# Performance work log

Hardware: AMD Instinct MI355X
Metric: run time of the kernel (lower is better)

Reference implementation:

```python
import jax, jax.numpy as jnp
import numpy as np

N, E, G, ND, H, C, L = 100000, 640000, 1000, 128, 128, 10, 4
ATOMS_PER_GRAPH = 100  # N = G * ATOMS_PER_GRAPH
NEG_SLOPE = 0.01  # nn.LeakyReLU default


def setup_inputs() -> dict:
    key = jax.random.key(0)
    ks = jax.random.split(key, 16)
    s = 0.05
    return {
        "node_attr": jax.random.normal(ks[0], (N, ND), jnp.float32),
        "edge_index": jax.random.randint(ks[1], (2, E), 0, N, jnp.int64),
        "num_atoms": jnp.full((G,), ATOMS_PER_GRAPH, dtype=jnp.int64),
        "enc_W": jax.random.normal(ks[2], (ND, H), jnp.float32) * s,
        "enc_b": jnp.zeros((H,), jnp.float32),
        "gcn_W": jax.random.normal(ks[3], (L, H, H), jnp.float32) * s,
        "gcn_b": jnp.zeros((L, H), jnp.float32),
        "r_W1": jax.random.normal(ks[4], (H, H), jnp.float32) * s,
        "r_b1": jnp.zeros((H,), jnp.float32),
        "r_W2": jax.random.normal(ks[5], (H, H), jnp.float32) * s,
        "r_b2": jnp.zeros((H,), jnp.float32),
        "s_W1": jax.random.normal(ks[6], (H, H), jnp.float32) * s,
        "s_b1": jnp.zeros((H,), jnp.float32),
        "s_W2": jax.random.normal(ks[7], (H, H), jnp.float32) * s,
        "s_b2": jnp.zeros((H,), jnp.float32),
        "fin_W": jax.random.normal(ks[8], (H, C), jnp.float32) * s,
        "fin_b": jnp.zeros((C,), jnp.float32),
    }


def _leaky(x):
    return jnp.where(x > 0, x, NEG_SLOPE * x)


def reference(node_attr, edge_index, num_atoms, enc_W, enc_b, gcn_W, gcn_b,
              r_W1, r_b1, r_W2, r_b2, s_W1, s_b1, s_W2, s_b2, fin_W, fin_b):
    dst, src = edge_index[0], edge_index[1]
    # degree normalization constant across layers: deg(i) = in-edge count, divide by deg+1
    deg = jax.ops.segment_sum(jnp.ones((E,), node_attr.dtype), dst, num_segments=N)
    inv_deg = 1.0 / (deg + 1.0)  # [N]

    x = node_attr @ enc_W + enc_b  # [N, H]
    for l in range(L):
        h = x @ gcn_W[l] + gcn_b[l]
        agg = jax.ops.segment_sum(h[src], dst, num_segments=N)  # scatter_sum over dst
        x = (h + agg) * inv_deg[:, None]

    # GateMLP: ReLuMLP(x) * SigmoidMLP(x)
    r = _leaky(_leaky(x @ r_W1 + r_b1) @ r_W2 + r_b2)
    g = jax.nn.sigmoid(_leaky(x @ s_W1 + s_b1) @ s_W2 + s_b2)
    x = r * g  # [N, H]

    # graph pooling: scatter_mean over graph ids
    graph_mask = jnp.repeat(jnp.arange(G), num_atoms, total_repeat_length=N)
    gsum = jax.ops.segment_sum(x, graph_mask, num_segments=G)
    cnt = jax.ops.segment_sum(jnp.ones((N,), x.dtype), graph_mask, num_segments=G)
    graph_attr = gsum / jnp.maximum(cnt, 1.0)[:, None]  # [G, H]
    return graph_attr @ fin_W + fin_b  # [G, C]
```

## Files before the change

kernel.cpp:

```cpp
#include <hip/hip_runtime.h>
#include <hip/hip_bf16.h>
#include <cstddef>
#include <cstdint>

#define CAP 40
#define LEAK 0.01f

typedef __attribute__((ext_vector_type(8))) short short8v;
typedef __attribute__((ext_vector_type(4))) float float4v;

__device__ __forceinline__ unsigned short f2bf(float f) {
    uint32_t u = __float_as_uint(f);
    uint32_t r = (u + 0x7FFFu + ((u >> 16) & 1u)) >> 16;
    return (unsigned short)r;
}
__device__ __forceinline__ float bf2f(unsigned short s) {
    return __uint_as_float(((uint32_t)s) << 16);
}
__device__ __forceinline__ short8v frag_from_pairs(uint32_t p0, uint32_t p1,
                                                   uint32_t p2, uint32_t p3) {
    union { uint32_t u[4]; short8v v; } c;
    c.u[0] = p0; c.u[1] = p1; c.u[2] = p2; c.u[3] = p3;
    return c.v;
}

__global__ void build_buckets(const int* __restrict__ ei, int E_,
                              int* __restrict__ cnt, int* __restrict__ bucket) {
    int e = (blockIdx.x * 256 + threadIdx.x) * 4;
    if (e >= E_) return;
    if (e + 4 <= E_) {
        int4 d4 = *(const int4*)&ei[e];
        int4 s4 = *(const int4*)&ei[(size_t)E_ + e];
        int p0 = atomicAdd(&cnt[d4.x], 1);
        int p1 = atomicAdd(&cnt[d4.y], 1);
        int p2 = atomicAdd(&cnt[d4.z], 1);
        int p3 = atomicAdd(&cnt[d4.w], 1);
        if (p0 < CAP) bucket[(size_t)d4.x * CAP + p0] = s4.x;
        if (p1 < CAP) bucket[(size_t)d4.y * CAP + p1] = s4.y;
        if (p2 < CAP) bucket[(size_t)d4.z * CAP + p2] = s4.z;
        if (p3 < CAP) bucket[(size_t)d4.w * CAP + p3] = s4.w;
    } else {
        for (; e < E_; ++e) {
            int d = ei[e], s = ei[(size_t)E_ + e];
            int p = atomicAdd(&cnt[d], 1);
            if (p < CAP) bucket[(size_t)d * CAP + p] = s;
        }
    }
}

__global__ void pack_w(const float* __restrict__ enc, const float* __restrict__ gcn,
                       const float* __restrict__ rw1, const float* __restrict__ rw2,
                       const float* __restrict__ sw1, const float* __restrict__ sw2,
                       unsigned short* __restrict__ p) {
    int m = blockIdx.x >> 3;
    int idx = (blockIdx.x & 7) * 256 + threadIdx.x;
    const float* W;
    switch (m) {
        case 0: W = enc; break;
        case 1: case 2: case 3: case 4: W = gcn + (size_t)(m - 1) * 16384; break;
        case 5: W = rw1; break;
        case 6: W = rw2; break;
        case 7: W = sw1; break;
        default: W = sw2; break;
    }
    int n = idx & 127;
    int fg = (idx >> 7) & 3;
    int kc = idx >> 9;
    short8v v;
#pragma unroll
    for (int j = 0; j < 8; ++j)
        v[j] = (short)f2bf(W[(size_t)(kc * 32 + fg * 8 + j) * 128 + n]);
    *(short8v*)(p + (size_t)m * 16384 + (size_t)idx * 8) = v;
}

__device__ __forceinline__ void load_wf(const unsigned short* __restrict__ Wpack,
                                        int w, int fr, int fg, short8v wf[2][4]) {
    const short8v* Wp = (const short8v*)Wpack;
#pragma unroll
    for (int t = 0; t < 2; ++t)
#pragma unroll
        for (int kc = 0; kc < 4; ++kc)
            wf[t][kc] = Wp[(kc * 4 + fg) * 128 + w * 32 + t * 16 + fr];
}

__device__ __forceinline__ void mfma_tile(const unsigned short* As, int fr, int fg,
                                          const short8v wf[2][4], float4v acc[4][2]) {
#pragma unroll
    for (int m = 0; m < 4; ++m) {
        acc[m][0] = (float4v){0.f, 0.f, 0.f, 0.f};
        acc[m][1] = (float4v){0.f, 0.f, 0.f, 0.f};
    }
#pragma unroll
    for (int kc = 0; kc < 4; ++kc) {
        short8v a[4];
#pragma unroll
        for (int m = 0; m < 4; ++m) {
            int row = m * 16 + fr;
            int cb = (kc * 64 + fg * 16) ^ ((row & 7) << 4);
            a[m] = *(const short8v*)((const char*)As + row * 256 + cb);
        }
#pragma unroll
        for (int m = 0; m < 4; ++m) {
            acc[m][0] = __builtin_amdgcn_mfma_f32_16x16x32_bf16(a[m], wf[0][kc], acc[m][0], 0, 0, 0);
            acc[m][1] = __builtin_amdgcn_mfma_f32_16x16x32_bf16(a[m], wf[1][kc], acc[m][1], 0, 0, 0);
        }
    }
}

__global__ __launch_bounds__(256) void gemm_enc(const float* __restrict__ Ain,
                                                const unsigned short* __restrict__ Wpack,
                                                const float* __restrict__ bias,
                                                unsigned short* __restrict__ Cout, int M) {
    __shared__ unsigned short As[64 * 128];
    const int tid = threadIdx.x;
    const int lane = tid & 63;
    const int w = tid >> 6;
    const int row0 = blockIdx.x * 64;
    const int fr = lane & 15;
    const int fg = lane >> 4;

    short8v wf[2][4];
    load_wf(Wpack, w, fr, fg, wf);

    {
        const int r = tid >> 2;
        const int cg = tid & 3;
        const int row = row0 + r;
        char* lbase = (char*)As + r * 256;
        const float* Ap = Ain + (size_t)row * 128 + cg * 32;
#pragma unroll
        for (int i = 0; i < 4; ++i) {
            short8v v = {0, 0, 0, 0, 0, 0, 0, 0};
            if (row < M) {
                float4v p = *(const float4v*)(Ap + i * 8);
                float4v q = *(const float4v*)(Ap + i * 8 + 4);
                v[0] = (short)f2bf(p[0]); v[1] = (short)f2bf(p[1]);
                v[2] = (short)f2bf(p[2]); v[3] = (short)f2bf(p[3]);
                v[4] = (short)f2bf(q[0]); v[5] = (short)f2bf(q[1]);
                v[6] = (short)f2bf(q[2]); v[7] = (short)f2bf(q[3]);
            }
            int cb = (cg * 64 + i * 16) ^ ((r & 7) << 4);
            *(short8v*)(lbase + cb) = v;
        }
    }
    __syncthreads();

    float4v acc[4][2];
    mfma_tile(As, fr, fg, wf, acc);

#pragma unroll
    for (int t = 0; t < 2; ++t) {
        const int col = w * 32 + t * 16 + fr;
        const float bv = bias[col];
#pragma unroll
        for (int m = 0; m < 4; ++m)
#pragma unroll
            for (int q = 0; q < 4; ++q) {
                int row = row0 + m * 16 + fg * 4 + q;
                if (row < M) Cout[(size_t)row * 128 + col] = f2bf(acc[m][t][q] + bv);
            }
    }
}

__device__ __forceinline__ void acc8(float a[8], uint4 v, float m) {
    a[0] = fmaf(m, bf2f((unsigned short)(v.x & 0xffff)), a[0]);
    a[1] = fmaf(m, bf2f((unsigned short)(v.x >> 16)), a[1]);
    a[2] = fmaf(m, bf2f((unsigned short)(v.y & 0xffff)), a[2]);
    a[3] = fmaf(m, bf2f((unsigned short)(v.y >> 16)), a[3]);
    a[4] = fmaf(m, bf2f((unsigned short)(v.z & 0xffff)), a[4]);
    a[5] = fmaf(m, bf2f((unsigned short)(v.z >> 16)), a[5]);
    a[6] = fmaf(m, bf2f((unsigned short)(v.w & 0xffff)), a[6]);
    a[7] = fmaf(m, bf2f((unsigned short)(v.w >> 16)), a[7]);
}

__global__ __launch_bounds__(256, 4) void gcn_fused(const unsigned short* __restrict__ x,
                                                    const int* __restrict__ bucket,
                                                    const int* __restrict__ cnt,
                                                    const unsigned short* __restrict__ Wpack,
                                                    const float* __restrict__ bias,
                                                    unsigned short* __restrict__ xout,
                                                    int Nn) {
    __shared__ unsigned short As[64 * 128];
    const int tid = threadIdx.x;
    const int lane = tid & 63;
    const int w = tid >> 6;
    const int row0 = blockIdx.x * 64;
    const int fr = lane & 15;
    const int fg = lane >> 4;
    const int l16 = lane & 15;
    const int g = lane >> 4;
    const int gl = lane & 48;
    const char* xb = (const char*)x;

    int cfull = 0;
    if (lane < 16) {
        int gn = row0 + w * 16 + lane;
        if (gn >= Nn) gn = Nn - 1;
        cfull = cnt[gn];
    }
    uint4 own[4];
    int2 pre[4];
#pragma unroll
    for (int p = 0; p < 4; ++p) {
        int gn = row0 + w * 16 + p * 4 + g;
        if (gn >= Nn) gn = Nn - 1;
        own[p] = *(const uint4*)(xb + (size_t)gn * 256 + l16 * 16);
        pre[p] = *(const int2*)&bucket[(size_t)gn * CAP + 2 * l16];
    }

#pragma unroll
    for (int p = 0; p < 4; ++p) {
        const int n = p * 4 + g;
        const int r = w * 16 + n;
        const int dfull = __shfl(cfull, n);
        const float id = 1.0f / (float)(dfull + 1);
        const int d = min(dfull, CAP);
        const int dm = min(d, 32);

        float a[8];
        {
            uint4 o = own[p];
            a[0] = bf2f((unsigned short)(o.x & 0xffff));
            a[1] = bf2f((unsigned short)(o.x >> 16));
            a[2] = bf2f((unsigned short)(o.y & 0xffff));
            a[3] = bf2f((unsigned short)(o.y >> 16));
            a[4] = bf2f((unsigned short)(o.z & 0xffff));
            a[5] = bf2f((unsigned short)(o.z >> 16));
            a[6] = bf2f((unsigned short)(o.w & 0xffff));
            a[7] = bf2f((unsigned short)(o.w >> 16));
        }

        for (int j = 0; j < dm; j += 4) {
            int sl = gl + (j >> 1);
            int s0 = __shfl(pre[p].x, sl);
            int s1 = __shfl(pre[p].y, sl);
            int s2 = __shfl(pre[p].x, sl + 1);
            int s3 = __shfl(pre[p].y, sl + 1);
            s0 = min(max(s0, 0), Nn - 1);
            s1 = min(max(s1, 0), Nn - 1);
            s2 = min(max(s2, 0), Nn - 1);
            s3 = min(max(s3, 0), Nn - 1);
            uint4 v0 = *(const uint4*)(xb + (size_t)s0 * 256 + l16 * 16);
            uint4 v1 = *(const uint4*)(xb + (size_t)s1 * 256 + l16 * 16);
            uint4 v2 = *(const uint4*)(xb + (size_t)s2 * 256 + l16 * 16);
            uint4 v3 = *(const uint4*)(xb + (size_t)s3 * 256 + l16 * 16);
            acc8(a, v0, (j + 0 < d) ? 1.f : 0.f);
            acc8(a, v1, (j + 1 < d) ? 1.f : 0.f);
            acc8(a, v2, (j + 2 < d) ? 1.f : 0.f);
            acc8(a, v3, (j + 3 < d) ? 1.f : 0.f);
        }
        if (d > 32) {
            int gn = row0 + r; if (gn >= Nn) gn = Nn - 1;
            for (int j = 32; j < d; ++j) {
                int s = bucket[(size_t)gn * CAP + j];
                uint4 v = *(const uint4*)(xb + (size_t)s * 256 + l16 * 16);
                acc8(a, v, 1.f);
            }
        }

#pragma unroll
        for (int i = 0; i < 8; ++i) a[i] *= id;
        uint4 o;
        o.x = (uint32_t)f2bf(a[0]) | ((uint32_t)f2bf(a[1]) << 16);
        o.y = (uint32_t)f2bf(a[2]) | ((uint32_t)f2bf(a[3]) << 16);
        o.z = (uint32_t)f2bf(a[4]) | ((uint32_t)f2bf(a[5]) << 16);
        o.w = (uint32_t)f2bf(a[6]) | ((uint32_t)f2bf(a[7]) << 16);
        *(uint4*)((char*)As + r * 256 + ((l16 * 16) ^ ((r & 7) << 4))) = o;
    }

    short8v wf[2][4];
    load_wf(Wpack, w, fr, fg, wf);
    __syncthreads();

    float4v acc[4][2];
    mfma_tile(As, fr, fg, wf, acc);

#pragma unroll
    for (int t = 0; t < 2; ++t) {
        const int col = w * 32 + t * 16 + fr;
        const float bv = bias[col];
#pragma unroll
        for (int m = 0; m < 4; ++m)
#pragma unroll
            for (int q = 0; q < 4; ++q) {
                int row = row0 + m * 16 + fg * 4 + q;
                if (row < Nn) xout[(size_t)row * 128 + col] = f2bf(acc[m][t][q] + bv);
            }
    }
}

__global__ __launch_bounds__(512, 4) void gate_fused(const unsigned short* __restrict__ x,
                                                     const unsigned short* __restrict__ wpack,
                                                     const float* __restrict__ rb1,
                                                     const float* __restrict__ rb2,
                                                     const float* __restrict__ sb1,
                                                     const float* __restrict__ sb2,
                                                     unsigned short* __restrict__ out, int M) {
    __shared__ unsigned short Ws[2 * 128 * 128];
    const int tid = threadIdx.x;
    const int lane = tid & 63;
    const int w = tid >> 6;
    const int l16 = lane & 15;
    const int fg = lane >> 4;
    const int row0 = blockIdx.x * 128 + w * 16;

    int xr = row0 + l16;
    if (xr >= M) xr = M - 1;
    short8v xbf[4];
#pragma unroll
    for (int kc = 0; kc < 4; ++kc)
        xbf[kc] = *(const short8v*)(x + (size_t)xr * 128 + kc * 32 + fg * 8);

    const short8v* WL = (const short8v*)Ws;
    uint32_t upR[8][2], upS[8][2];

#define STAGE2(mi0, mi1)                                                      \
    {                                                                         \
        const short8v* s0 = (const short8v*)(wpack + (size_t)(mi0) * 16384);  \
        const short8v* s1 = (const short8v*)(wpack + (size_t)(mi1) * 16384);  \
        short8v* dst = (short8v*)Ws;                                          \
        _Pragma("unroll") for (int i = 0; i < 4; ++i)                         \
            dst[i * 512 + tid] = s0[i * 512 + tid];                           \
        _Pragma("unroll") for (int i = 0; i < 4; ++i)                         \
            dst[2048 + i * 512 + tid] = s1[i * 512 + tid];                    \
    }

#define PASS1(OFS, BIAS, UP)                                                  \
    _Pragma("unroll") for (int nt = 0; nt < 8; ++nt) {                        \
        float4v acc = (float4v){0.f, 0.f, 0.f, 0.f};                          \
        _Pragma("unroll") for (int kc = 0; kc < 4; ++kc)                      \
            acc = __builtin_amdgcn_mfma_f32_16x16x32_bf16(                    \
                WL[(OFS) + (kc * 4 + fg) * 128 + nt * 16 + l16], xbf[kc], acc, 0, 0, 0); \
        _Pragma("unroll") for (int q = 0; q < 4; ++q) {                       \
            float v = acc[q] + (BIAS)[nt * 16 + fg * 4 + q];                  \
            acc[q] = v > 0.f ? v : LEAK * v;                                  \
        }                                                                     \
        UP[nt][0] = (uint32_t)f2bf(acc[0]) | ((uint32_t)f2bf(acc[1]) << 16);  \
        UP[nt][1] = (uint32_t)f2bf(acc[2]) | ((uint32_t)f2bf(acc[3]) << 16);  \
    }

#define MKUF(UP, UF)                                                          \
    _Pragma("unroll") for (int kc = 0; kc < 4; ++kc) {                        \
        uint32_t pr0, pr1, pr2, pr3;                                          \
        {                                                                     \
            int srcl = (((2 * fg + 0) & 3) << 4) + l16;                       \
            uint32_t lo = __shfl((int)UP[2 * kc][0], srcl);                   \
            uint32_t hi = __shfl((int)UP[2 * kc + 1][0], srcl);               \
            pr0 = (fg & 2) ? hi : lo;                                         \
            lo = __shfl((int)UP[2 * kc][1], srcl);                            \
            hi = __shfl((int)UP[2 * kc + 1][1], srcl);                        \
            pr1 = (fg & 2) ? hi : lo;                                         \
        }                                                                     \
        {                                                                     \
            int srcl = (((2 * fg + 1) & 3) << 4) + l16;                       \
            uint32_t lo = __shfl((int)UP[2 * kc][0], srcl);                   \
            uint32_t hi = __shfl((int)UP[2 * kc + 1][0], srcl);               \
            pr2 = (fg & 2) ? hi : lo;                                         \
            lo = __shfl((int)UP[2 * kc][1], srcl);                            \
            hi = __shfl((int)UP[2 * kc + 1][1], srcl);                        \
            pr3 = (fg & 2) ? hi : lo;                                         \
        }                                                                     \
        UF[kc] = frag_from_pairs(pr0, pr1, pr2, pr3);                         \
    }

    STAGE2(5, 7);
    __syncthreads();
    PASS1(0, rb1, upR);
    PASS1(2048, sb1, upS);
    __syncthreads();

    STAGE2(6, 8);
    __syncthreads();

    short8v uf[4];
    MKUF(upR, uf);
    float4v rf[8];
#pragma unroll
    for (int t2 = 0; t2 < 8; ++t2) {
        float4v acc = (float4v){0.f, 0.f, 0.f, 0.f};
#pragma unroll
        for (int kc = 0; kc < 4; ++kc)
            acc = __builtin_amdgcn_mfma_f32_16x16x32_bf16(
                uf[kc], WL[(kc * 4 + fg) * 128 + t2 * 16 + l16], acc, 0, 0, 0);
        const float bv = rb2[t2 * 16 + l16];
#pragma unroll
        for (int q = 0; q < 4; ++q) {
            float v = acc[q] + bv;
            rf[t2][q] = v > 0.f ? v : LEAK * v;
        }
    }

    MKUF(upS, uf);
#pragma unroll
    for (int t2 = 0; t2 < 8; ++t2) {
        float4v acc = (float4v){0.f, 0.f, 0.f, 0.f};
#pragma unroll
        for (int kc = 0; kc < 4; ++kc)
            acc = __builtin_amdgcn_mfma_f32_16x16x32_bf16(
                uf[kc], WL[2048 + (kc * 4 + fg) * 128 + t2 * 16 + l16], acc, 0, 0, 0);
        const float bv = sb2[t2 * 16 + l16];
#pragma unroll
        for (int q = 0; q < 4; ++q) {
            int row = row0 + fg * 4 + q;
            if (row < M) {
                float gg = 1.f / (1.f + __expf(-(acc[q] + bv)));
                out[(size_t)row * 128 + t2 * 16 + l16] = f2bf(gg * rf[t2][q]);
            }
        }
    }
#undef STAGE2
#undef PASS1
#undef MKUF
}

__global__ void scan_atoms(const int* __restrict__ na, int* __restrict__ goff, int G_) {
    __shared__ int sh[1024];
    int t = threadIdx.x;
    int v = (t < G_) ? na[t] : 0;
    sh[t] = v;
    __syncthreads();
    for (int ofs = 1; ofs < 1024; ofs <<= 1) {
        int u = (t >= ofs) ? sh[t - ofs] : 0;
        __syncthreads();
        sh[t] += u;
        __syncthreads();
    }
    if (t == 0) goff[0] = 0;
    if (t < G_) goff[t + 1] = sh[t];
}

__global__ void pool(const unsigned short* __restrict__ x, const int* __restrict__ goff,
                     float* __restrict__ gattr, int G_) {
    int g = blockIdx.x * 2 + (threadIdx.x >> 7);
    if (g >= G_) return;
    int d = threadIdx.x & 127;
    int a0 = goff[g], a1 = goff[g + 1];
    float s0 = 0.f, s1 = 0.f, s2 = 0.f, s3 = 0.f;
    int a = a0;
    for (; a + 4 <= a1; a += 4) {
        s0 += bf2f(x[(size_t)(a + 0) * 128 + d]);
        s1 += bf2f(x[(size_t)(a + 1) * 128 + d]);
        s2 += bf2f(x[(size_t)(a + 2) * 128 + d]);
        s3 += bf2f(x[(size_t)(a + 3) * 128 + d]);
    }
    for (; a < a1; ++a) s0 += bf2f(x[(size_t)a * 128 + d]);
    float s = (s0 + s1) + (s2 + s3);
    float c = (float)max(a1 - a0, 1);
    gattr[(size_t)g * 128 + d] = s / c;
}

__global__ void final_gemm(const float* __restrict__ gattr, const float* __restrict__ fW,
                           const float* __restrict__ fb, float* __restrict__ out,
                           int G_, int C_) {
    int i = blockIdx.x * 256 + threadIdx.x;
    if (i >= G_ * C_) return;
    int g = i / C_, c = i % C_;
    const float* row = gattr + (size_t)g * 128;
    float s = fb[c];
    for (int k = 0; k < 128; ++k) s = fmaf(row[k], fW[k * C_ + c], s);
    out[i] = s;
}

extern "C" void kernel_launch(void* const* d_in, const int* in_sizes, int n_in,
                              void* d_out, int out_size, void* d_ws, size_t ws_size,
                              hipStream_t stream) {
    const float* node_attr = (const float*)d_in[0];
    const int* edge_index  = (const int*)d_in[1];
    const int* num_atoms   = (const int*)d_in[2];
    const float* enc_W = (const float*)d_in[3];
    const float* enc_b = (const float*)d_in[4];
    const float* gcn_W = (const float*)d_in[5];
    const float* gcn_b = (const float*)d_in[6];
    const float* r_W1 = (const float*)d_in[7];
    const float* r_b1 = (const float*)d_in[8];
    const float* r_W2 = (const float*)d_in[9];
    const float* r_b2 = (const float*)d_in[10];
    const float* s_W1 = (const float*)d_in[11];
    const float* s_b1 = (const float*)d_in[12];
    const float* s_W2 = (const float*)d_in[13];
    const float* s_b2 = (const float*)d_in[14];
    const float* fin_W = (const float*)d_in[15];
    const float* fin_b = (const float*)d_in[16];
    float* out = (float*)d_out;

    const int N_ = in_sizes[0] / 128;
    const int E_ = in_sizes[1] / 2;
    const int G_ = in_sizes[2];
    const int C_ = in_sizes[16];

    size_t off = 0;
    auto alloc = [&](size_t bytes) -> void* {
        void* p = (char*)d_ws + off;
        off += (bytes + 255) & ~(size_t)255;
        return p;
    };
    unsigned short* bx = (unsigned short*)alloc((size_t)N_ * 128 * 2);
    unsigned short* bh = (unsigned short*)alloc((size_t)N_ * 128 * 2);
    int* bucket = (int*)alloc((size_t)N_ * CAP * 4);
    int* cnt    = (int*)alloc((size_t)N_ * 4);
    unsigned short* wpack = (unsigned short*)alloc((size_t)9 * 16384 * 2);
    int* goff   = (int*)alloc((size_t)(G_ + 1) * 4);
    float* gattr = (float*)alloc((size_t)G_ * 128 * 4);
    (void)ws_size; (void)n_in; (void)out_size;

    const int gemm_grid = (N_ + 63) / 64;

    hipMemsetAsync(cnt, 0, (size_t)N_ * 4, stream);
    build_buckets<<<(E_ / 4 + 255) / 256, 256, 0, stream>>>(edge_index, E_, cnt, bucket);
    pack_w<<<72, 256, 0, stream>>>(enc_W, gcn_W, r_W1, r_W2, s_W1, s_W2, wpack);
    scan_atoms<<<1, 1024, 0, stream>>>(num_atoms, goff, G_);

    gemm_enc<<<gemm_grid, 256, 0, stream>>>(node_attr, wpack, enc_b, bx, N_);

    unsigned short* cur = bx;
    unsigned short* nxt = bh;
    for (int l = 0; l < 4; ++l) {
        gcn_fused<<<gemm_grid, 256, 0, stream>>>(cur, bucket, cnt,
                                                 wpack + (size_t)(1 + l) * 16384,
                                                 gcn_b + (size_t)l * 128, nxt, N_);
        unsigned short* t = cur; cur = nxt; nxt = t;
    }

    gate_fused<<<(N_ + 127) / 128, 512, 0, stream>>>(cur, wpack, r_b1, r_b2, s_b1, s_b2,
                                                     nxt, N_);

    pool<<<(G_ + 1) / 2, 256, 0, stream>>>(nxt, goff, gattr, G_);
    final_gemm<<<(G_ * C_ + 255) / 256, 256, 0, stream>>>(gattr, fin_W, fin_b, out, G_, C_);
}
```

Measured before the change: 297.5 us.

## Fold encoder and last GCN weights into adjacent GEMMs, merge prep kernels

Aggregation and degree normalisation are linear, so they commute with the right-multiply by the weights. This change folds the encoder weight into the first GCN layer weight, and the last GCN weight into the first gate-MLP weights, with the biases folded to match. The encoder GEMM kernel goes away, and the last GCN layer only aggregates before writing. Bucket building, node_attr bf16 conversion, weight packing and the small weight-product matmuls now run in one combined prep launch. The cost is extra prep work and bf16 rounding of the products, which changes numerics slightly.

```diff
diff --git a/kernel.cpp b/kernel.cpp
--- a/kernel.cpp
+++ b/kernel.cpp
@@ -24,53 +24,113 @@
     return c.v;
 }
 
-__global__ void build_buckets(const int* __restrict__ ei, int E_,
-                              int* __restrict__ cnt, int* __restrict__ bucket) {
-    int e = (blockIdx.x * 256 + threadIdx.x) * 4;
-    if (e >= E_) return;
-    if (e + 4 <= E_) {
-        int4 d4 = *(const int4*)&ei[e];
-        int4 s4 = *(const int4*)&ei[(size_t)E_ + e];
-        int p0 = atomicAdd(&cnt[d4.x], 1);
-        int p1 = atomicAdd(&cnt[d4.y], 1);
-        int p2 = atomicAdd(&cnt[d4.z], 1);
-        int p3 = atomicAdd(&cnt[d4.w], 1);
-        if (p0 < CAP) bucket[(size_t)d4.x * CAP + p0] = s4.x;
-        if (p1 < CAP) bucket[(size_t)d4.y * CAP + p1] = s4.y;
-        if (p2 < CAP) bucket[(size_t)d4.z * CAP + p2] = s4.z;
-        if (p3 < CAP) bucket[(size_t)d4.w * CAP + p3] = s4.w;
-    } else {
-        for (; e < E_; ++e) {
-            int d = ei[e], s = ei[(size_t)E_ + e];
-            int p = atomicAdd(&cnt[d], 1);
-            if (p < CAP) bucket[(size_t)d * CAP + p] = s;
-        }
-    }
-}
-
-__global__ void pack_w(const float* __restrict__ enc, const float* __restrict__ gcn,
-                       const float* __restrict__ rw1, const float* __restrict__ rw2,
-                       const float* __restrict__ sw1, const float* __restrict__ sw2,
-                       unsigned short* __restrict__ p) {
-    int m = blockIdx.x >> 3;
-    int idx = (blockIdx.x & 7) * 256 + threadIdx.x;
-    const float* W;
-    switch (m) {
-        case 0: W = enc; break;
-        case 1: case 2: case 3: case 4: W = gcn + (size_t)(m - 1) * 16384; break;
-        case 5: W = rw1; break;
-        case 6: W = rw2; break;
-        case 7: W = sw1; break;
-        default: W = sw2; break;
-    }
-    int n = idx & 127;
-    int fg = (idx >> 7) & 3;
-    int kc = idx >> 9;
-    short8v v;
-#pragma unroll
-    for (int j = 0; j < 8; ++j)
-        v[j] = (short)f2bf(W[(size_t)(kc * 32 + fg * 8 + j) * 128 + n]);
-    *(short8v*)(p + (size_t)m * 16384 + (size_t)idx * 8) = v;
+__global__ __launch_bounds__(256) void prep(const int* __restrict__ ei, int E_,
+                                            int* __restrict__ cnt,
+                                            int* __restrict__ bucket,
+                                            const float* __restrict__ node_attr,
+                                            unsigned short* __restrict__ bx, int Nn,
+                                            const float* __restrict__ enc_W,
+                                            const float* __restrict__ gcn_W,
+                                            const float* __restrict__ rw1,
+                                            const float* __restrict__ rw2,
+                                            const float* __restrict__ sw1,
+                                            const float* __restrict__ sw2,
+                                            const float* __restrict__ enc_b,
+                                            const float* __restrict__ gcn_b,
+                                            const float* __restrict__ rb1,
+                                            const float* __restrict__ sb1,
+                                            unsigned short* __restrict__ wpack,
+                                            float* __restrict__ fbias,
+                                            int NB_EDGE, int NB_CVT) {
+    const int b = blockIdx.x;
+    const int tid = threadIdx.x;
+
+    if (b < NB_EDGE) {
+        int e = (b * 256 + tid) * 4;
+        if (e >= E_) return;
+        if (e + 4 <= E_) {
+            int4 d4 = *(const int4*)&ei[e];
+            int4 s4 = *(const int4*)&ei[(size_t)E_ + e];
+            int p0 = atomicAdd(&cnt[d4.x], 1);
+            int p1 = atomicAdd(&cnt[d4.y], 1);
+            int p2 = atomicAdd(&cnt[d4.z], 1);
+            int p3 = atomicAdd(&cnt[d4.w], 1);
+            if (p0 < CAP) bucket[(size_t)d4.x * CAP + p0] = s4.x;
+            if (p1 < CAP) bucket[(size_t)d4.y * CAP + p1] = s4.y;
+            if (p2 < CAP) bucket[(size_t)d4.z * CAP + p2] = s4.z;
+            if (p3 < CAP) bucket[(size_t)d4.w * CAP + p3] = s4.w;
+        } else {
+            for (; e < E_; ++e) {
+                int d = ei[e], s = ei[(size_t)E_ + e];
+                int p = atomicAdd(&cnt[d], 1);
+                if (p < CAP) bucket[(size_t)d * CAP + p] = s;
+            }
+        }
+        return;
+    }
+    if (b < NB_EDGE + NB_CVT) {
+        size_t i8 = ((size_t)(b - NB_EDGE) * 256 + tid) * 8;
+        if (i8 < (size_t)Nn * 128) {
+            const float* ap = node_attr + i8;
+            float4v p = *(const float4v*)ap;
+            float4v q = *(const float4v*)(ap + 4);
+            short8v v;
+            v[0] = (short)f2bf(p[0]); v[1] = (short)f2bf(p[1]);
+            v[2] = (short)f2bf(p[2]); v[3] = (short)f2bf(p[3]);
+            v[4] = (short)f2bf(q[0]); v[5] = (short)f2bf(q[1]);
+            v[6] = (short)f2bf(q[2]); v[7] = (short)f2bf(q[3]);
+            *(short8v*)(bx + i8) = v;
+        }
+        return;
+    }
+    if (b < NB_EDGE + NB_CVT + 72) {
+        int pb = b - (NB_EDGE + NB_CVT);
+        int m = pb >> 3;
+        if (m == 1) return;
+        int idx = (pb & 7) * 256 + tid;
+        const float* W;
+        switch (m) {
+            case 0: W = enc_W; break;
+            case 2: case 3: case 4: W = gcn_W + (size_t)(m - 1) * 16384; break;
+            case 5: W = rw1; break;
+            case 6: W = rw2; break;
+            case 7: W = sw1; break;
+            default: W = sw2; break;
+        }
+        int n = idx & 127;
+        int fg = (idx >> 7) & 3;
+        int kc = idx >> 9;
+        short8v v;
+#pragma unroll
+        for (int j = 0; j < 8; ++j)
+            v[j] = (short)f2bf(W[(size_t)(kc * 32 + fg * 8 + j) * 128 + n]);
+        *(short8v*)(wpack + (size_t)m * 16384 + (size_t)idx * 8) = v;
+        return;
+    }
+    int fb = b - (NB_EDGE + NB_CVT + 72);
+    if (fb < 192) {
+        int which = fb / 64;
+        int r = (fb % 64) * 2 + (tid >> 7);
+        int n = tid & 127;
+        const float* A = (which == 0) ? enc_W : gcn_W + (size_t)3 * 16384;
+        const float* B = (which == 0) ? gcn_W : ((which == 1) ? rw1 : sw1);
+        float acc = 0.f;
+#pragma unroll 8
+        for (int m2 = 0; m2 < 128; ++m2)
+            acc = fmaf(A[(size_t)r * 128 + m2], B[(size_t)m2 * 128 + n], acc);
+        int kc = r >> 5, fg2 = (r >> 3) & 3, j = r & 7;
+        int sl = (which == 0) ? 1 : ((which == 1) ? 9 : 10);
+        wpack[(size_t)sl * 16384 + (size_t)(((kc * 4 + fg2) * 128 + n) * 8 + j)] = f2bf(acc);
+    } else if (fb < 195 && tid < 128) {
+        int which = fb - 192;
+        const float* B = (which == 0) ? gcn_W : ((which == 1) ? rw1 : sw1);
+        const float* ba = (which == 0) ? enc_b : gcn_b + 384;
+        const float* bb = (which == 0) ? gcn_b : ((which == 1) ? rb1 : sb1);
+        float acc = bb[tid];
+        for (int m2 = 0; m2 < 128; ++m2)
+            acc = fmaf(ba[m2], B[(size_t)m2 * 128 + tid], acc);
+        fbias[which * 128 + tid] = acc;
+    }
 }
 
 __device__ __forceinline__ void load_wf(const unsigned short* __restrict__ Wpack,
@@ -104,61 +164,6 @@
             acc[m][0] = __builtin_amdgcn_mfma_f32_16x16x32_bf16(a[m], wf[0][kc], acc[m][0], 0, 0, 0);
             acc[m][1] = __builtin_amdgcn_mfma_f32_16x16x32_bf16(a[m], wf[1][kc], acc[m][1], 0, 0, 0);
         }
-    }
-}
-
-__global__ __launch_bounds__(256) void gemm_enc(const float* __restrict__ Ain,
-                                                const unsigned short* __restrict__ Wpack,
-                                                const float* __restrict__ bias,
-                                                unsigned short* __restrict__ Cout, int M) {
-    __shared__ unsigned short As[64 * 128];
-    const int tid = threadIdx.x;
-    const int lane = tid & 63;
-    const int w = tid >> 6;
-    const int row0 = blockIdx.x * 64;
-    const int fr = lane & 15;
-    const int fg = lane >> 4;
-
-    short8v wf[2][4];
-    load_wf(Wpack, w, fr, fg, wf);
-
-    {
-        const int r = tid >> 2;
-        const int cg = tid & 3;
-        const int row = row0 + r;
-        char* lbase = (char*)As + r * 256;
-        const float* Ap = Ain + (size_t)row * 128 + cg * 32;
-#pragma unroll
-        for (int i = 0; i < 4; ++i) {
-            short8v v = {0, 0, 0, 0, 0, 0, 0, 0};
-            if (row < M) {
-                float4v p = *(const float4v*)(Ap + i * 8);
-                float4v q = *(const float4v*)(Ap + i * 8 + 4);
-                v[0] = (short)f2bf(p[0]); v[1] = (short)f2bf(p[1]);
-                v[2] = (short)f2bf(p[2]); v[3] = (short)f2bf(p[3]);
-                v[4] = (short)f2bf(q[0]); v[5] = (short)f2bf(q[1]);
-                v[6] = (short)f2bf(q[2]); v[7] = (short)f2bf(q[3]);
-            }
-            int cb = (cg * 64 + i * 16) ^ ((r & 7) << 4);
-            *(short8v*)(lbase + cb) = v;
-        }
-    }
-    __syncthreads();
-
-    float4v acc[4][2];
-    mfma_tile(As, fr, fg, wf, acc);
-
-#pragma unroll
-    for (int t = 0; t < 2; ++t) {
-        const int col = w * 32 + t * 16 + fr;
-        const float bv = bias[col];
-#pragma unroll
-        for (int m = 0; m < 4; ++m)
-#pragma unroll
-            for (int q = 0; q < 4; ++q) {
-                int row = row0 + m * 16 + fg * 4 + q;
-                if (row < M) Cout[(size_t)row * 128 + col] = f2bf(acc[m][t][q] + bv);
-            }
     }
 }
 
@@ -173,6 +178,7 @@
     a[7] = fmaf(m, bf2f((unsigned short)(v.w >> 16)), a[7]);
 }
 
+template <bool AGGONLY>
 __global__ __launch_bounds__(256, 4) void gcn_fused(const unsigned short* __restrict__ x,
                                                     const int* __restrict__ bucket,
                                                     const int* __restrict__ cnt,
@@ -265,8 +271,15 @@
         o.y = (uint32_t)f2bf(a[2]) | ((uint32_t)f2bf(a[3]) << 16);
         o.z = (uint32_t)f2bf(a[4]) | ((uint32_t)f2bf(a[5]) << 16);
         o.w = (uint32_t)f2bf(a[6]) | ((uint32_t)f2bf(a[7]) << 16);
-        *(uint4*)((char*)As + r * 256 + ((l16 * 16) ^ ((r & 7) << 4))) = o;
-    }
+        if (AGGONLY) {
+            int node = row0 + r;
+            if (node < Nn)
+                *(uint4*)((char*)xout + (size_t)node * 256 + l16 * 16) = o;
+        } else {
+            *(uint4*)((char*)As + r * 256 + ((l16 * 16) ^ ((r & 7) << 4))) = o;
+        }
+    }
+    if (AGGONLY) return;
 
     short8v wf[2][4];
     load_wf(Wpack, w, fr, fg, wf);
@@ -291,9 +304,9 @@
 
 __global__ __launch_bounds__(512, 4) void gate_fused(const unsigned short* __restrict__ x,
                                                      const unsigned short* __restrict__ wpack,
-                                                     const float* __restrict__ rb1,
+                                                     const float* __restrict__ rb1f,
                                                      const float* __restrict__ rb2,
-                                                     const float* __restrict__ sb1,
+                                                     const float* __restrict__ sb1f,
                                                      const float* __restrict__ sb2,
                                                      unsigned short* __restrict__ out, int M) {
     __shared__ unsigned short Ws[2 * 128 * 128];
@@ -320,7 +333,7 @@
         const short8v* s1 = (const short8v*)(wpack + (size_t)(mi1) * 16384);  \
         short8v* dst = (short8v*)Ws;                                          \
         _Pragma("unroll") for (int i = 0; i < 4; ++i)                         \
-            dst[i * 512 + tid] = s0[i * 512 + tid];                           \
+            dst[i * 512 + tid] = s0[i * 512 + tid];                          \
         _Pragma("unroll") for (int i = 0; i < 4; ++i)                         \
             dst[2048 + i * 512 + tid] = s1[i * 512 + tid];                    \
     }
@@ -363,10 +376,10 @@
         UF[kc] = frag_from_pairs(pr0, pr1, pr2, pr3);                         \
     }
 
-    STAGE2(5, 7);
+    STAGE2(9, 10);
     __syncthreads();
-    PASS1(0, rb1, upR);
-    PASS1(2048, sb1, upS);
+    PASS1(0, rb1f, upR);
+    PASS1(2048, sb1f, upS);
     __syncthreads();
 
     STAGE2(6, 8);
@@ -498,32 +511,37 @@
     unsigned short* bh = (unsigned short*)alloc((size_t)N_ * 128 * 2);
     int* bucket = (int*)alloc((size_t)N_ * CAP * 4);
     int* cnt    = (int*)alloc((size_t)N_ * 4);
-    unsigned short* wpack = (unsigned short*)alloc((size_t)9 * 16384 * 2);
+    unsigned short* wpack = (unsigned short*)alloc((size_t)11 * 16384 * 2);
+    float* fbias = (float*)alloc((size_t)3 * 128 * 4);
     int* goff   = (int*)alloc((size_t)(G_ + 1) * 4);
     float* gattr = (float*)alloc((size_t)G_ * 128 * 4);
     (void)ws_size; (void)n_in; (void)out_size;
 
     const int gemm_grid = (N_ + 63) / 64;
+    const int NB_EDGE = (E_ / 4 + 255) / 256;
+    const int NB_CVT = (N_ * 16 + 255) / 256;
+    const int NB_PREP = NB_EDGE + NB_CVT + 72 + 195;
 
     hipMemsetAsync(cnt, 0, (size_t)N_ * 4, stream);
-    build_buckets<<<(E_ / 4 + 255) / 256, 256, 0, stream>>>(edge_index, E_, cnt, bucket);
-    pack_w<<<72, 256, 0, stream>>>(enc_W, gcn_W, r_W1, r_W2, s_W1, s_W2, wpack);
+    prep<<<NB_PREP, 256, 0, stream>>>(edge_index, E_, cnt, bucket,
+                                      node_attr, bx, N_,
+                                      enc_W, gcn_W, r_W1, r_W2, s_W1, s_W2,
+                                      enc_b, gcn_b, r_b1, s_b1,
+                                      wpack, fbias, NB_EDGE, NB_CVT);
     scan_atoms<<<1, 1024, 0, stream>>>(num_atoms, goff, G_);
 
-    gemm_enc<<<gemm_grid, 256, 0, stream>>>(node_attr, wpack, enc_b, bx, N_);
-
-    unsigned short* cur = bx;
-    unsigned short* nxt = bh;
-    for (int l = 0; l < 4; ++l) {
-        gcn_fused<<<gemm_grid, 256, 0, stream>>>(cur, bucket, cnt,
-                                                 wpack + (size_t)(1 + l) * 16384,
-                                                 gcn_b + (size_t)l * 128, nxt, N_);
-        unsigned short* t = cur; cur = nxt; nxt = t;
-    }
-
-    gate_fused<<<(N_ + 127) / 128, 512, 0, stream>>>(cur, wpack, r_b1, r_b2, s_b1, s_b2,
-                                                     nxt, N_);
-
-    pool<<<(G_ + 1) / 2, 256, 0, stream>>>(nxt, goff, gattr, G_);
+    gcn_fused<false><<<gemm_grid, 256, 0, stream>>>(bx, bucket, cnt,
+                                                    wpack + (size_t)1 * 16384, fbias, bh, N_);
+    gcn_fused<false><<<gemm_grid, 256, 0, stream>>>(bh, bucket, cnt,
+                                                    wpack + (size_t)2 * 16384, gcn_b + 128, bx, N_);
+    gcn_fused<false><<<gemm_grid, 256, 0, stream>>>(bx, bucket, cnt,
+                                                    wpack + (size_t)3 * 16384, gcn_b + 256, bh, N_);
+    gcn_fused<true><<<gemm_grid, 256, 0, stream>>>(bh, bucket, cnt,
+                                                   wpack + (size_t)4 * 16384, nullptr, bx, N_);
+
+    gate_fused<<<(N_ + 127) / 128, 512, 0, stream>>>(bx, wpack, fbias + 128, r_b2,
+                                                     fbias + 256, s_b2, bh, N_);
+
+    pool<<<(G_ + 1) / 2, 256, 0, stream>>>(bh, goff, gattr, G_);
     final_gemm<<<(G_ * C_ + 255) / 256, 256, 0, stream>>>(gattr, fin_W, fin_b, out, G_, C_);
 }
```

After: 277.7 us. 1.07x faster.
